# Performance work log

Hardware: AMD Instinct MI355X
Metric: run time of the kernel (lower is better)

Reference implementation:

```python
import jax, jax.numpy as jnp
import numpy as np

N = 50000      # nodes
D = 128        # in_dim
O = 128        # out_dim
MAX_DEG = 32   # degrees uniform in [0, MAX_DEG]


def setup_inputs() -> dict:
    rng = np.random.default_rng(0)
    deg = rng.integers(0, MAX_DEG + 1, size=N)          # includes deg==0 nodes
    dst = np.repeat(np.arange(N), deg)                  # target node per edge (grouped, like the buckets)
    E = dst.shape[0]                                    # ~800000
    src = rng.integers(0, N, size=E)                    # neighbor index per edge (flat neighbor_list)

    key = jax.random.key(0)
    k1, k2, k3, k4 = jax.random.split(key, 4)
    scale = jnp.float32(1.0 / np.sqrt(D))
    return {
        "x":  jax.random.normal(k1, (N, D), jnp.float32),
        "Wg": jax.random.normal(k2, (O, D), jnp.float32) * scale,  # global_lin.weight
        "Wl": jax.random.normal(k3, (O, D), jnp.float32) * scale,  # local_lin.weight
        "Ws": jax.random.normal(k4, (O, D), jnp.float32) * scale,  # self_lin.weight
        "b":  jnp.zeros((O,), jnp.float32),                        # bias param
        "src": jnp.asarray(src, jnp.int32),
        "dst": jnp.asarray(dst, jnp.int32),
        "deg": jnp.asarray(deg, jnp.int32),
    }


def reference(x, Wg, Wl, Ws, b, src, dst, deg):
    n = x.shape[0]
    # global branch: applied to every node
    g_out = x @ Wg.T                                           # [N, O]
    # mean-aggregate neighbor features (gather + segment-sum == the per-bucket view().mean())
    neigh_sum = jax.ops.segment_sum(x[src], dst, num_segments=n)   # [N, D]
    degf = jnp.maximum(deg, 1).astype(x.dtype)[:, None]
    neigh_mean = neigh_sum * (1.0 / degf)                       # [N, D]
    # local + self branches only for deg > 0 (deg==0 bucket keeps just global_out)
    mask = (deg > 0).astype(x.dtype)[:, None]                   # [N, 1]
    out = g_out + mask * (neigh_mean @ Wl.T + x @ Ws.T) + b
    # dropout is identity in eval mode; ELU activation
    return jax.nn.elu(out)
```

## Files before the change

### kernel.cpp

```cpp
#include <hip/hip_runtime.h>
#include <cstdint>
#include <cstddef>

#define KCAT 384
#define GNPB 8
#define MNPB 16
#define GAST 264
#define VP_BLOCKS 24

typedef __attribute__((ext_vector_type(8))) short bf16x8;
typedef __attribute__((ext_vector_type(4))) float f32x4;

static __device__ __forceinline__ unsigned short f2bf(float f) {
    unsigned int u = __builtin_bit_cast(unsigned int, f);
    u += 0x7fffu + ((u >> 16) & 1u);
    return (unsigned short)(u >> 16);
}
static __device__ __forceinline__ float bfhi(unsigned int u) { return __builtin_bit_cast(float, u & 0xFFFF0000u); }
static __device__ __forceinline__ float bflo(unsigned int u) { return __builtin_bit_cast(float, u << 16); }
static __device__ __forceinline__ void acc8(float* a, const uint4& v, unsigned m) {
    unsigned x0 = v.x & m, x1 = v.y & m, x2 = v.z & m, x3 = v.w & m;
    a[0] += bflo(x0); a[1] += bfhi(x0); a[2] += bflo(x1); a[3] += bfhi(x1);
    a[4] += bflo(x2); a[5] += bfhi(x2); a[6] += bflo(x3); a[7] += bfhi(x3);
}

__global__ __launch_bounds__(256)
void prep(const float* __restrict__ x, const float* __restrict__ Wg,
          const float* __restrict__ Wl, const float* __restrict__ Ws,
          const int* __restrict__ dst, unsigned short* __restrict__ Vp,
          unsigned short* __restrict__ xb, int* __restrict__ blkoff,
          int total8, int nblk_g, int noffb, int E) {
    const int bx = blockIdx.x, t = threadIdx.x;
    if (bx < VP_BLOCKS) {
        int gid = bx * 256 + t;
        if (gid < 6144) {
            int l = gid & 63, srow = (gid >> 6) % 12, g = gid / 768;
            int o = g * 16 + (l & 15);
            int k = srow * 32 + (l >> 4) * 8;
            const float* w; int kk;
            if (k < 128)      { w = Wg; kk = k; }
            else if (k < 256) { w = Wl; kk = k - 128; }
            else              { w = Ws; kk = k - 256; }
            const float* p = w + o * 128 + kk;
            uint4 u;
            u.x = (unsigned)f2bf(p[0]) | ((unsigned)f2bf(p[1]) << 16);
            u.y = (unsigned)f2bf(p[2]) | ((unsigned)f2bf(p[3]) << 16);
            u.z = (unsigned)f2bf(p[4]) | ((unsigned)f2bf(p[5]) << 16);
            u.w = (unsigned)f2bf(p[6]) | ((unsigned)f2bf(p[7]) << 16);
            ((uint4*)Vp)[gid] = u;
        }
    } else if (bx < VP_BLOCKS + noffb) {
        int b = (bx - VP_BLOCKS) * 256 + t;
        if (b < nblk_g) {
            int target = b * GNPB;
            int lo = 0, hi = E;
            while (lo < hi) { int mid = (lo + hi) >> 1; if (dst[mid] < target) lo = mid + 1; else hi = mid; }
            blkoff[b] = lo;
        }
    } else {
        int gid = (bx - VP_BLOCKS - noffb) * 256 + t;
        if (gid < total8) {
            const float4* px = (const float4*)x + (size_t)gid * 2;
            float4 a = px[0], bq = px[1];
            uint4 u;
            u.x = (unsigned)f2bf(a.x)  | ((unsigned)f2bf(a.y)  << 16);
            u.y = (unsigned)f2bf(a.z)  | ((unsigned)f2bf(a.w)  << 16);
            u.z = (unsigned)f2bf(bq.x) | ((unsigned)f2bf(bq.y) << 16);
            u.w = (unsigned)f2bf(bq.z) | ((unsigned)f2bf(bq.w) << 16);
            ((uint4*)xb)[gid] = u;
        }
    }
}

__global__ __launch_bounds__(512, 7)
void gather(const unsigned short* __restrict__ xb, const int* __restrict__ src,
            const int* __restrict__ deg, const int* __restrict__ blkoff,
            unsigned short* __restrict__ M, int N) {
    const int t = threadIdx.x, wv = t >> 6, lane = t & 63;
    const int c = lane & 15, p = lane >> 4;
    const int base = blockIdx.x * GNPB;

    int dg8 = 0;
    if (lane < GNPB && base + lane < N) dg8 = deg[base + lane];
    int incl = dg8;
#pragma unroll
    for (int off = 1; off < GNPB; off <<= 1) {
        int v = __shfl_up(incl, off, 64);
        if (lane >= off) incl += v;
    }
    const int d = __shfl(dg8, wv, 64);
    const int s = blkoff[blockIdx.x] + __shfl(incl, wv, 64) - d;
    const int n = base + wv;
    if (n >= N) return;

    int idx = 0;
    if (lane < d) idx = src[s + lane];

    const uint4* x4 = (const uint4*)xb;
    int r0 = __shfl(idx, p, 64),      r1 = __shfl(idx, p + 4, 64);
    int r2 = __shfl(idx, p + 8, 64),  r3 = __shfl(idx, p + 12, 64);
    uint4 v0 = x4[(size_t)r0 * 16 + c], v1 = x4[(size_t)r1 * 16 + c];
    uint4 v2 = x4[(size_t)r2 * 16 + c], v3 = x4[(size_t)r3 * 16 + c];
    uint4 v4, v5, v6, v7;
    const bool two = (d > 16);
    if (two) {
        int e = 16 + p;
        int r4 = __shfl(idx, e, 64),      r5 = __shfl(idx, e + 4, 64);
        int r6 = __shfl(idx, e + 8, 64),  r7 = __shfl(idx, e + 12, 64);
        v4 = x4[(size_t)r4 * 16 + c]; v5 = x4[(size_t)r5 * 16 + c];
        v6 = x4[(size_t)r6 * 16 + c]; v7 = x4[(size_t)r7 * 16 + c];
    }
    float a[8] = {0,0,0,0,0,0,0,0};
    float b[8] = {0,0,0,0,0,0,0,0};
    acc8(a, v0, (p      < d) ? ~0u : 0u);
    acc8(b, v1, (p + 4  < d) ? ~0u : 0u);
    acc8(a, v2, (p + 8  < d) ? ~0u : 0u);
    acc8(b, v3, (p + 12 < d) ? ~0u : 0u);
    if (two) {
        int e = 16 + p;
        acc8(a, v4, (e      < d) ? ~0u : 0u);
        acc8(b, v5, (e + 4  < d) ? ~0u : 0u);
        acc8(a, v6, (e + 8  < d) ? ~0u : 0u);
        acc8(b, v7, (e + 12 < d) ? ~0u : 0u);
    }
#pragma unroll
    for (int i = 0; i < 8; ++i) a[i] += b[i];
#pragma unroll
    for (int i = 0; i < 8; ++i) {
        a[i] += __shfl_xor(a[i], 16, 64);
        a[i] += __shfl_xor(a[i], 32, 64);
    }
    if (p == 0) {
        float inv = (d > 0) ? 1.0f / (float)d : 0.0f;
        uint4 u;
        u.x = (unsigned)f2bf(a[0]*inv) | ((unsigned)f2bf(a[1]*inv) << 16);
        u.y = (unsigned)f2bf(a[2]*inv) | ((unsigned)f2bf(a[3]*inv) << 16);
        u.z = (unsigned)f2bf(a[4]*inv) | ((unsigned)f2bf(a[5]*inv) << 16);
        u.w = (unsigned)f2bf(a[6]*inv) | ((unsigned)f2bf(a[7]*inv) << 16);
        ((uint4*)M)[(size_t)n * 16 + c] = u;
    }
}

__global__ __launch_bounds__(256)
void gemm(const unsigned short* __restrict__ xb, const unsigned short* __restrict__ Mm,
          const int* __restrict__ deg, const unsigned short* __restrict__ Vp,
          const float* __restrict__ bias, float* __restrict__ out, int N) {
    __shared__ __align__(16) unsigned short As[MNPB * GAST];
    __shared__ unsigned smask[MNPB];
    const int t = threadIdx.x, wv = t >> 6, lane = t & 63;
    const int c = lane & 15, quad = lane >> 4;
    const int base = blockIdx.x * MNPB;

    if (t < MNPB) smask[t] = (base + t < N && deg[base + t] > 0) ? 0xFFFFFFFFu : 0u;
#pragma unroll
    for (int it = 0; it < 2; ++it) {
        int f = it * 256 + t;
        int row = f >> 5, ch = f & 31;
        int grow = base + row; if (grow > N - 1) grow = N - 1;
        const unsigned short* gp = (ch < 16)
            ? xb + (size_t)grow * 128 + ch * 8
            : Mm + (size_t)grow * 128 + (ch - 16) * 8;
        uint4 val = *(const uint4*)gp;
        *(uint4*)(As + row * GAST + ch * 8) = val;
    }
    __syncthreads();

    const unsigned msk = smask[c];
    const int g0 = 2 * wv, g1 = 2 * wv + 1;
    const bf16x8* VB = (const bf16x8*)Vp;

    f32x4 acc0 = (f32x4){0.f, 0.f, 0.f, 0.f};
    f32x4 acc1 = (f32x4){0.f, 0.f, 0.f, 0.f};
    bf16x8 b0 = VB[(g0 * 12) * 64 + lane];
    bf16x8 b1 = VB[(g1 * 12) * 64 + lane];
#pragma unroll
    for (int s2 = 0; s2 < 12; ++s2) {
        int sn = (s2 + 1 < 12) ? s2 + 1 : 0;
        bf16x8 n0 = VB[(g0 * 12 + sn) * 64 + lane];
        bf16x8 n1 = VB[(g1 * 12 + sn) * 64 + lane];
        int seg = s2 >> 2, kk = (s2 & 3) * 32;
        bf16x8 a0 = *(const bf16x8*)(As + c * GAST + (seg == 1 ? 128 : 0) + kk + quad * 8);
        if (seg == 2) {
            uint4 ai = __builtin_bit_cast(uint4, a0);
            ai.x &= msk; ai.y &= msk; ai.z &= msk; ai.w &= msk;
            a0 = __builtin_bit_cast(bf16x8, ai);
        }
        acc0 = __builtin_amdgcn_mfma_f32_16x16x32_bf16(a0, b0, acc0, 0, 0, 0);
        acc1 = __builtin_amdgcn_mfma_f32_16x16x32_bf16(a0, b1, acc1, 0, 0, 0);
        b0 = n0; b1 = n1;
    }

    const int col0 = g0 * 16 + c, col1 = g1 * 16 + c;
    const float bv0 = bias[col0], bv1 = bias[col1];
#pragma unroll
    for (int reg = 0; reg < 4; ++reg) {
        int grow = base + quad * 4 + reg;
        if (grow < N) {
            float v0 = acc0[reg] + bv0;
            float v1 = acc1[reg] + bv1;
            out[(size_t)grow * 128 + col0] = (v0 > 0.f) ? v0 : __expf(v0) - 1.0f;
            out[(size_t)grow * 128 + col1] = (v1 > 0.f) ? v1 : __expf(v1) - 1.0f;
        }
    }
}

extern "C" void kernel_launch(void* const* d_in, const int* in_sizes, int n_in,
                              void* d_out, int out_size, void* d_ws, size_t ws_size,
                              hipStream_t stream) {
    const float* x  = (const float*)d_in[0];
    const float* Wg = (const float*)d_in[1];
    const float* Wl = (const float*)d_in[2];
    const float* Ws = (const float*)d_in[3];
    const float* b  = (const float*)d_in[4];
    const int*   src = (const int*)d_in[5];
    const int*   dst = (const int*)d_in[6];
    const int*   deg = (const int*)d_in[7];
    const int E = in_sizes[5];
    const int N = in_sizes[7];
    float* out = (float*)d_out;

    const size_t NB = (size_t)N * 128 * 2;
    unsigned short* Vp     = (unsigned short*)d_ws;
    int*            blkoff = (int*)((char*)d_ws + 98304);
    unsigned short* xb     = (unsigned short*)((char*)d_ws + 131072);
    unsigned short* Mm     = (unsigned short*)((char*)d_ws + 131072 + NB);

    const int nblk_g = (N + GNPB - 1) / GNPB;
    const int noffb  = (nblk_g + 255) / 256;
    const int total8 = N * 16;
    const int nconv  = (total8 + 255) / 256;

    prep<<<dim3(VP_BLOCKS + noffb + nconv), dim3(256), 0, stream>>>(
        x, Wg, Wl, Ws, dst, Vp, xb, blkoff, total8, nblk_g, noffb, E);
    gather<<<dim3(nblk_g), dim3(512), 0, stream>>>(xb, src, deg, blkoff, Mm, N);
    gemm<<<dim3((N + MNPB - 1) / MNPB), dim3(256), 0, stream>>>(xb, Mm, deg, Vp, b, out, N);
}
```

Baseline: 142.0 us.

## Fuse neighbor gather into GEMM, fold Wg+Ws, fix deg-zero nodes separately

Merges the gather and GEMM kernels so each block first computes the mean neighbor features for its 16 nodes directly into shared memory. This avoids writing and re-reading the intermediate M buffer in global memory. The Wg and Ws weights are pre-summed, shrinking K from 384 to 256 and dropping the mask work from the MFMA loop. Nodes with degree zero then get wrong values (Ws is still applied), so a small extra kernel recomputes their output from x@Wg in fp32. The costs are one more launch, lower occupancy per block, and serial per-node gathering within each wave.

```diff
diff --git a/kernel.cpp b/kernel.cpp
--- a/kernel.cpp
+++ b/kernel.cpp
@@ -2,11 +2,10 @@
 #include <cstdint>
 #include <cstddef>
 
-#define KCAT 384
-#define GNPB 8
+#define GNPB 16
 #define MNPB 16
 #define GAST 264
-#define VP_BLOCKS 24
+#define VP_BLOCKS 16
 
 typedef __attribute__((ext_vector_type(8))) short bf16x8;
 typedef __attribute__((ext_vector_type(4))) float f32x4;
@@ -33,20 +32,25 @@
     const int bx = blockIdx.x, t = threadIdx.x;
     if (bx < VP_BLOCKS) {
         int gid = bx * 256 + t;
-        if (gid < 6144) {
-            int l = gid & 63, srow = (gid >> 6) % 12, g = gid / 768;
+        if (gid < 4096) {
+            int l = gid & 63, srow = (gid >> 6) & 7, g = gid >> 9;
             int o = g * 16 + (l & 15);
             int k = srow * 32 + (l >> 4) * 8;
-            const float* w; int kk;
-            if (k < 128)      { w = Wg; kk = k; }
-            else if (k < 256) { w = Wl; kk = k - 128; }
-            else              { w = Ws; kk = k - 256; }
-            const float* p = w + o * 128 + kk;
             uint4 u;
-            u.x = (unsigned)f2bf(p[0]) | ((unsigned)f2bf(p[1]) << 16);
-            u.y = (unsigned)f2bf(p[2]) | ((unsigned)f2bf(p[3]) << 16);
-            u.z = (unsigned)f2bf(p[4]) | ((unsigned)f2bf(p[5]) << 16);
-            u.w = (unsigned)f2bf(p[6]) | ((unsigned)f2bf(p[7]) << 16);
+            if (k < 128) {
+                const float* pg = Wg + o * 128 + k;
+                const float* ps = Ws + o * 128 + k;
+                u.x = (unsigned)f2bf(pg[0]+ps[0]) | ((unsigned)f2bf(pg[1]+ps[1]) << 16);
+                u.y = (unsigned)f2bf(pg[2]+ps[2]) | ((unsigned)f2bf(pg[3]+ps[3]) << 16);
+                u.z = (unsigned)f2bf(pg[4]+ps[4]) | ((unsigned)f2bf(pg[5]+ps[5]) << 16);
+                u.w = (unsigned)f2bf(pg[6]+ps[6]) | ((unsigned)f2bf(pg[7]+ps[7]) << 16);
+            } else {
+                const float* pl = Wl + o * 128 + (k - 128);
+                u.x = (unsigned)f2bf(pl[0]) | ((unsigned)f2bf(pl[1]) << 16);
+                u.y = (unsigned)f2bf(pl[2]) | ((unsigned)f2bf(pl[3]) << 16);
+                u.z = (unsigned)f2bf(pl[4]) | ((unsigned)f2bf(pl[5]) << 16);
+                u.w = (unsigned)f2bf(pl[6]) | ((unsigned)f2bf(pl[7]) << 16);
+            }
             ((uint4*)Vp)[gid] = u;
         }
     } else if (bx < VP_BLOCKS + noffb) {
@@ -72,119 +76,99 @@
     }
 }
 
-__global__ __launch_bounds__(512, 7)
-void gather(const unsigned short* __restrict__ xb, const int* __restrict__ src,
-            const int* __restrict__ deg, const int* __restrict__ blkoff,
-            unsigned short* __restrict__ M, int N) {
+__global__ __launch_bounds__(256, 5)
+void fused(const unsigned short* __restrict__ xb, const int* __restrict__ src,
+           const int* __restrict__ deg, const int* __restrict__ blkoff,
+           const unsigned short* __restrict__ Vp, const float* __restrict__ bias,
+           float* __restrict__ out, int N) {
+    __shared__ __align__(16) unsigned short As[MNPB * GAST];
     const int t = threadIdx.x, wv = t >> 6, lane = t & 63;
     const int c = lane & 15, p = lane >> 4;
     const int base = blockIdx.x * GNPB;
 
-    int dg8 = 0;
-    if (lane < GNPB && base + lane < N) dg8 = deg[base + lane];
-    int incl = dg8;
-#pragma unroll
-    for (int off = 1; off < GNPB; off <<= 1) {
+    const int srow = t >> 4, sch = t & 15;
+    int sgrow = base + srow; if (sgrow > N - 1) sgrow = N - 1;
+    const uint4 sval = *(const uint4*)(xb + (size_t)sgrow * 128 + sch * 8);
+
+    int dg16 = 0;
+    if (lane < 16 && base + lane < N) dg16 = deg[base + lane];
+    int incl = dg16;
+#pragma unroll
+    for (int off = 1; off < 16; off <<= 1) {
         int v = __shfl_up(incl, off, 64);
         if (lane >= off) incl += v;
     }
-    const int d = __shfl(dg8, wv, 64);
-    const int s = blkoff[blockIdx.x] + __shfl(incl, wv, 64) - d;
-    const int n = base + wv;
-    if (n >= N) return;
-
-    int idx = 0;
-    if (lane < d) idx = src[s + lane];
+    const int blk_s = blkoff[blockIdx.x];
 
     const uint4* x4 = (const uint4*)xb;
-    int r0 = __shfl(idx, p, 64),      r1 = __shfl(idx, p + 4, 64);
-    int r2 = __shfl(idx, p + 8, 64),  r3 = __shfl(idx, p + 12, 64);
-    uint4 v0 = x4[(size_t)r0 * 16 + c], v1 = x4[(size_t)r1 * 16 + c];
-    uint4 v2 = x4[(size_t)r2 * 16 + c], v3 = x4[(size_t)r3 * 16 + c];
-    uint4 v4, v5, v6, v7;
-    const bool two = (d > 16);
-    if (two) {
-        int e = 16 + p;
-        int r4 = __shfl(idx, e, 64),      r5 = __shfl(idx, e + 4, 64);
-        int r6 = __shfl(idx, e + 8, 64),  r7 = __shfl(idx, e + 12, 64);
-        v4 = x4[(size_t)r4 * 16 + c]; v5 = x4[(size_t)r5 * 16 + c];
-        v6 = x4[(size_t)r6 * 16 + c]; v7 = x4[(size_t)r7 * 16 + c];
-    }
-    float a[8] = {0,0,0,0,0,0,0,0};
-    float b[8] = {0,0,0,0,0,0,0,0};
-    acc8(a, v0, (p      < d) ? ~0u : 0u);
-    acc8(b, v1, (p + 4  < d) ? ~0u : 0u);
-    acc8(a, v2, (p + 8  < d) ? ~0u : 0u);
-    acc8(b, v3, (p + 12 < d) ? ~0u : 0u);
-    if (two) {
-        int e = 16 + p;
-        acc8(a, v4, (e      < d) ? ~0u : 0u);
-        acc8(b, v5, (e + 4  < d) ? ~0u : 0u);
-        acc8(a, v6, (e + 8  < d) ? ~0u : 0u);
-        acc8(b, v7, (e + 12 < d) ? ~0u : 0u);
-    }
-#pragma unroll
-    for (int i = 0; i < 8; ++i) a[i] += b[i];
-#pragma unroll
-    for (int i = 0; i < 8; ++i) {
-        a[i] += __shfl_xor(a[i], 16, 64);
-        a[i] += __shfl_xor(a[i], 32, 64);
-    }
-    if (p == 0) {
-        float inv = (d > 0) ? 1.0f / (float)d : 0.0f;
-        uint4 u;
-        u.x = (unsigned)f2bf(a[0]*inv) | ((unsigned)f2bf(a[1]*inv) << 16);
-        u.y = (unsigned)f2bf(a[2]*inv) | ((unsigned)f2bf(a[3]*inv) << 16);
-        u.z = (unsigned)f2bf(a[4]*inv) | ((unsigned)f2bf(a[5]*inv) << 16);
-        u.w = (unsigned)f2bf(a[6]*inv) | ((unsigned)f2bf(a[7]*inv) << 16);
-        ((uint4*)M)[(size_t)n * 16 + c] = u;
-    }
-}
-
-__global__ __launch_bounds__(256)
-void gemm(const unsigned short* __restrict__ xb, const unsigned short* __restrict__ Mm,
-          const int* __restrict__ deg, const unsigned short* __restrict__ Vp,
-          const float* __restrict__ bias, float* __restrict__ out, int N) {
-    __shared__ __align__(16) unsigned short As[MNPB * GAST];
-    __shared__ unsigned smask[MNPB];
-    const int t = threadIdx.x, wv = t >> 6, lane = t & 63;
-    const int c = lane & 15, quad = lane >> 4;
-    const int base = blockIdx.x * MNPB;
-
-    if (t < MNPB) smask[t] = (base + t < N && deg[base + t] > 0) ? 0xFFFFFFFFu : 0u;
-#pragma unroll
-    for (int it = 0; it < 2; ++it) {
-        int f = it * 256 + t;
-        int row = f >> 5, ch = f & 31;
-        int grow = base + row; if (grow > N - 1) grow = N - 1;
-        const unsigned short* gp = (ch < 16)
-            ? xb + (size_t)grow * 128 + ch * 8
-            : Mm + (size_t)grow * 128 + (ch - 16) * 8;
-        uint4 val = *(const uint4*)gp;
-        *(uint4*)(As + row * GAST + ch * 8) = val;
-    }
-    __syncthreads();
-
-    const unsigned msk = smask[c];
+#pragma unroll 1
+    for (int i = 0; i < 4; ++i) {
+        const int j = (wv << 2) | i;
+        const int d = __shfl(dg16, j, 64);
+        const int s = blk_s + __shfl(incl, j, 64) - d;
+        float a[8] = {0,0,0,0,0,0,0,0};
+        if (d > 0) {
+            int idx = 0;
+            if (lane < d) idx = src[s + lane];
+            int r0 = __shfl(idx, p, 64),      r1 = __shfl(idx, p + 4, 64);
+            int r2 = __shfl(idx, p + 8, 64),  r3 = __shfl(idx, p + 12, 64);
+            uint4 v0 = x4[(size_t)r0 * 16 + c], v1 = x4[(size_t)r1 * 16 + c];
+            uint4 v2 = x4[(size_t)r2 * 16 + c], v3 = x4[(size_t)r3 * 16 + c];
+            uint4 v4, v5, v6, v7;
+            const bool two = (d > 16);
+            if (two) {
+                int e = 16 + p;
+                int r4 = __shfl(idx, e, 64),      r5 = __shfl(idx, e + 4, 64);
+                int r6 = __shfl(idx, e + 8, 64),  r7 = __shfl(idx, e + 12, 64);
+                v4 = x4[(size_t)r4 * 16 + c]; v5 = x4[(size_t)r5 * 16 + c];
+                v6 = x4[(size_t)r6 * 16 + c]; v7 = x4[(size_t)r7 * 16 + c];
+            }
+            float b[8] = {0,0,0,0,0,0,0,0};
+            acc8(a, v0, (p      < d) ? ~0u : 0u);
+            acc8(b, v1, (p + 4  < d) ? ~0u : 0u);
+            acc8(a, v2, (p + 8  < d) ? ~0u : 0u);
+            acc8(b, v3, (p + 12 < d) ? ~0u : 0u);
+            if (two) {
+                int e = 16 + p;
+                acc8(a, v4, (e      < d) ? ~0u : 0u);
+                acc8(b, v5, (e + 4  < d) ? ~0u : 0u);
+                acc8(a, v6, (e + 8  < d) ? ~0u : 0u);
+                acc8(b, v7, (e + 12 < d) ? ~0u : 0u);
+            }
+#pragma unroll
+            for (int q = 0; q < 8; ++q) a[q] += b[q];
+#pragma unroll
+            for (int q = 0; q < 8; ++q) {
+                a[q] += __shfl_xor(a[q], 16, 64);
+                a[q] += __shfl_xor(a[q], 32, 64);
+            }
+        }
+        if (p == 0) {
+            float inv = (d > 0) ? 1.0f / (float)d : 0.0f;
+            uint4 u;
+            u.x = (unsigned)f2bf(a[0]*inv) | ((unsigned)f2bf(a[1]*inv) << 16);
+            u.y = (unsigned)f2bf(a[2]*inv) | ((unsigned)f2bf(a[3]*inv) << 16);
+            u.z = (unsigned)f2bf(a[4]*inv) | ((unsigned)f2bf(a[5]*inv) << 16);
+            u.w = (unsigned)f2bf(a[6]*inv) | ((unsigned)f2bf(a[7]*inv) << 16);
+            *(uint4*)(As + j * GAST + 128 + c * 8) = u;
+        }
+    }
+
+    *(uint4*)(As + srow * GAST + sch * 8) = sval;
     const int g0 = 2 * wv, g1 = 2 * wv + 1;
     const bf16x8* VB = (const bf16x8*)Vp;
+    bf16x8 b0 = VB[(g0 * 8) * 64 + lane];
+    bf16x8 b1 = VB[(g1 * 8) * 64 + lane];
+    __syncthreads();
 
     f32x4 acc0 = (f32x4){0.f, 0.f, 0.f, 0.f};
     f32x4 acc1 = (f32x4){0.f, 0.f, 0.f, 0.f};
-    bf16x8 b0 = VB[(g0 * 12) * 64 + lane];
-    bf16x8 b1 = VB[(g1 * 12) * 64 + lane];
-#pragma unroll
-    for (int s2 = 0; s2 < 12; ++s2) {
-        int sn = (s2 + 1 < 12) ? s2 + 1 : 0;
-        bf16x8 n0 = VB[(g0 * 12 + sn) * 64 + lane];
-        bf16x8 n1 = VB[(g1 * 12 + sn) * 64 + lane];
-        int seg = s2 >> 2, kk = (s2 & 3) * 32;
-        bf16x8 a0 = *(const bf16x8*)(As + c * GAST + (seg == 1 ? 128 : 0) + kk + quad * 8);
-        if (seg == 2) {
-            uint4 ai = __builtin_bit_cast(uint4, a0);
-            ai.x &= msk; ai.y &= msk; ai.z &= msk; ai.w &= msk;
-            a0 = __builtin_bit_cast(bf16x8, ai);
-        }
+#pragma unroll
+    for (int s2 = 0; s2 < 8; ++s2) {
+        int sn = (s2 + 1 < 8) ? s2 + 1 : 0;
+        bf16x8 n0 = VB[(g0 * 8 + sn) * 64 + lane];
+        bf16x8 n1 = VB[(g1 * 8 + sn) * 64 + lane];
+        bf16x8 a0 = *(const bf16x8*)(As + c * GAST + s2 * 32 + p * 8);
         acc0 = __builtin_amdgcn_mfma_f32_16x16x32_bf16(a0, b0, acc0, 0, 0, 0);
         acc1 = __builtin_amdgcn_mfma_f32_16x16x32_bf16(a0, b1, acc1, 0, 0, 0);
         b0 = n0; b1 = n1;
@@ -194,13 +178,45 @@
     const float bv0 = bias[col0], bv1 = bias[col1];
 #pragma unroll
     for (int reg = 0; reg < 4; ++reg) {
-        int grow = base + quad * 4 + reg;
+        int grow = base + p * 4 + reg;
         if (grow < N) {
             float v0 = acc0[reg] + bv0;
             float v1 = acc1[reg] + bv1;
             out[(size_t)grow * 128 + col0] = (v0 > 0.f) ? v0 : __expf(v0) - 1.0f;
             out[(size_t)grow * 128 + col1] = (v1 > 0.f) ? v1 : __expf(v1) - 1.0f;
         }
+    }
+}
+
+__global__ __launch_bounds__(256)
+void degfix(const float* __restrict__ x, const float* __restrict__ Wg,
+            const float* __restrict__ bias, const int* __restrict__ deg,
+            float* __restrict__ out, int N) {
+    const int t = threadIdx.x, lane = t & 63;
+    const int nb = blockIdx.x * 256 + t;
+    int d = 1;
+    if (nb < N) d = deg[nb];
+    unsigned long long m = __ballot(d == 0);
+    const int wbase = blockIdx.x * 256 + ((t >> 6) << 6);
+    while (m) {
+        int bit = __builtin_ctzll(m);
+        m &= m - 1;
+        int n = wbase + bit;
+        const float* xr = x + (size_t)n * 128;
+        const float* w0 = Wg + (size_t)lane * 128;
+        const float* w1 = Wg + (size_t)(lane + 64) * 128;
+        float a0 = 0.f, a1 = 0.f;
+#pragma unroll 8
+        for (int k = 0; k < 128; k += 4) {
+            float4 xv = *(const float4*)(xr + k);
+            float4 wa = *(const float4*)(w0 + k);
+            float4 wb = *(const float4*)(w1 + k);
+            a0 += xv.x * wa.x + xv.y * wa.y + xv.z * wa.z + xv.w * wa.w;
+            a1 += xv.x * wb.x + xv.y * wb.y + xv.z * wb.z + xv.w * wb.w;
+        }
+        a0 += bias[lane]; a1 += bias[lane + 64];
+        out[(size_t)n * 128 + lane]      = (a0 > 0.f) ? a0 : __expf(a0) - 1.0f;
+        out[(size_t)n * 128 + lane + 64] = (a1 > 0.f) ? a1 : __expf(a1) - 1.0f;
     }
 }
 
@@ -219,11 +235,9 @@
     const int N = in_sizes[7];
     float* out = (float*)d_out;
 
-    const size_t NB = (size_t)N * 128 * 2;
     unsigned short* Vp     = (unsigned short*)d_ws;
-    int*            blkoff = (int*)((char*)d_ws + 98304);
-    unsigned short* xb     = (unsigned short*)((char*)d_ws + 131072);
-    unsigned short* Mm     = (unsigned short*)((char*)d_ws + 131072 + NB);
+    int*            blkoff = (int*)((char*)d_ws + 65536);
+    unsigned short* xb     = (unsigned short*)((char*)d_ws + 98304);
 
     const int nblk_g = (N + GNPB - 1) / GNPB;
     const int noffb  = (nblk_g + 255) / 256;
@@ -232,6 +246,6 @@
 
     prep<<<dim3(VP_BLOCKS + noffb + nconv), dim3(256), 0, stream>>>(
         x, Wg, Wl, Ws, dst, Vp, xb, blkoff, total8, nblk_g, noffb, E);
-    gather<<<dim3(nblk_g), dim3(512), 0, stream>>>(xb, src, deg, blkoff, Mm, N);
-    gemm<<<dim3((N + MNPB - 1) / MNPB), dim3(256), 0, stream>>>(xb, Mm, deg, Vp, b, out, N);
-}
+    fused<<<dim3(nblk_g), dim3(256), 0, stream>>>(xb, src, deg, blkoff, Vp, b, out, N);
+    degfix<<<dim3((N + 255) / 256), dim3(256), 0, stream>>>(x, Wg, b, deg, out, N);
+}
```

New measurement: 174.1 us. 22.6% more time.
